# Performance work log

Hardware: AMD Instinct MI355X
Metric: run time of the kernel (lower is better)

## Reference

```python
import jax, jax.numpy as jnp
from jax import lax
import numpy as np

K = 8          # local window radius -> (2K+1)^2 = 289 offsets
TOPK = 256     # topk channels kept for fg/bg correlation
EPS = 1e-5     # torch InstanceNorm2d default eps


def _conv3(x, w, b):
    # 3x3 conv, stride 1, pad 1, NCHW/OIHW
    y = lax.conv_general_dilated(x, w, (1, 1), ((1, 1), (1, 1)),
                                 dimension_numbers=('NCHW', 'OIHW', 'NCHW'))
    return y + b[None, :, None, None]


def _inorm(x):
    # InstanceNorm2d(affine=False): per (b,c) normalization over HxW, biased var
    m = jnp.mean(x, axis=(2, 3), keepdims=True)
    v = jnp.mean((x - m) ** 2, axis=(2, 3), keepdims=True)
    return (x - m) * lax.rsqrt(v + EPS)


def _aic(x, w1, b1, w2, b2):
    # AIC(in, hidden): conv3x3(in->hidden)+IN+ReLU -> conv3x3(hidden->in)+IN+ReLU
    h = jax.nn.relu(_inorm(_conv3(x, w1, b1)))
    return jax.nn.relu(_inorm(_conv3(h, w2, b2)))


def _amaxpool(x, H, W):
    # adaptive_max_pool2d with exact integer factor (384/48 = 8)
    kh, kw = x.shape[2] // H, x.shape[3] // W
    return lax.reduce_window(x, -jnp.inf, lax.max, (1, 1, kh, kw), (1, 1, kh, kw), 'VALID')


def _topk_c(x, k=TOPK):
    # topk over channel axis, values sorted descending (matches torch.topk)
    v, _ = lax.top_k(jnp.transpose(x, (0, 2, 3, 1)), k)  # [B,H,W,k]
    return jnp.transpose(v, (0, 3, 1, 2))                 # [B,k,H,W]


def _resize_ac(x, H, W):
    # bilinear interpolate, align_corners=True
    B, C, h, w = x.shape
    def grid(n_out, n_in):
        if n_out == 1:
            return jnp.zeros((1,), jnp.float32)
        return jnp.arange(n_out, dtype=jnp.float32) * ((n_in - 1) / (n_out - 1))
    ys, xs = grid(H, h), grid(W, w)
    y0 = jnp.clip(jnp.floor(ys).astype(jnp.int32), 0, h - 1)
    y1 = jnp.minimum(y0 + 1, h - 1)
    x0 = jnp.clip(jnp.floor(xs).astype(jnp.int32), 0, w - 1)
    x1 = jnp.minimum(x0 + 1, w - 1)
    wy = (ys - y0.astype(jnp.float32))[None, None, :, None]
    wx = (xs - x0.astype(jnp.float32))[None, None, None, :]
    rows = x[:, :, y0, :] * (1.0 - wy) + x[:, :, y1, :] * wy  # [B,C,H,w]
    return rows[:, :, :, x0] * (1.0 - wx) + rows[:, :, :, x1] * wx


def _forward(p3, p2, p1, kg1, klp, key_mask, pre_mask,
             conv_top_w, conv_top_b,
             aic_top_w1, aic_top_b1, aic_top_w2, aic_top_b2,
             r1a_w1, r1a_b1, r1a_w2, r1a_b2,
             r1b_w1, r1b_b1, r1b_w2, r1b_b2,
             r2a_w1, r2a_b1, r2a_w2, r2a_b2,
             r2b_w1, r2b_b1, r2b_w2, r2b_b2,
             dec_conv1_w, dec_conv1_b, pred_w, pred_b):
    B, _, H, W = kg1.shape  # kg1: [B, H*W, H, W]
    # --- Global, mode=2: fg/bg topk over the global correlation volume ---
    gm = _amaxpool(key_mask, H, W).reshape(B, H * W, 1, 1)
    gf = _topk_c(kg1 * gm)
    gb = _topk_c(kg1 * (1.0 - gm))
    # --- Local, mode=2: unfold mask into 17x17 windows, fg/bg topk ---
    lm = _amaxpool(pre_mask, H, W)                       # [B,1,H,W]
    lmp = jnp.pad(lm, ((0, 0), (0, 0), (K, K), (K, K)))  # zero pad (FF.pad default)
    patches = lax.conv_general_dilated_patches(
        lmp, (2 * K + 1, 2 * K + 1), (1, 1), 'VALID',
        dimension_numbers=('NCHW', 'OIHW', 'NCHW'))      # [B,289,H,W], ch = dy*17+dx
    lf = _topk_c(klp * patches)
    lb = _topk_c(klp * (1.0 - patches))
    # --- fuse at p3 resolution ---
    pm = _amaxpool(pre_mask, H, W)
    x = jnp.concatenate([p3, gf, gb, lf, lb, pm], axis=1)  # [B, 256*5+1, H, W]
    x = _conv3(x, conv_top_w, conv_top_b)                  # 1281 -> 256
    x = _aic(x, aic_top_w1, aic_top_b1, aic_top_w2, aic_top_b2)
    # --- Decoder: Refine(256,64) -> conv 256->64 -> Refine(64,64) -> pred ---
    y = _resize_ac(x, p2.shape[2], p2.shape[3])
    y = _aic(y, r1a_w1, r1a_b1, r1a_w2, r1a_b2)
    y = y + p2
    y = _aic(y, r1b_w1, r1b_b1, r1b_w2, r1b_b2)
    y = _conv3(y, dec_conv1_w, dec_conv1_b)
    z = _resize_ac(y, p1.shape[2], p1.shape[3])
    z = _aic(z, r2a_w1, r2a_b1, r2a_w2, r2a_b2)
    z = z + p1
    z = _aic(z, r2b_w1, r2b_b1, r2b_w2, r2b_b2)
    return jax.nn.sigmoid(_conv3(z, pred_w, pred_b))       # [B,1,192,192]


def setup_inputs() -> dict:
    key = jax.random.key(0)
    ks = jax.random.split(key, 40)
    B, H, W = 2, 48, 48
    inp = {}
    inp['p3'] = jax.random.normal(ks[0], (B, 256, H, W), jnp.float32)
    inp['p2'] = jax.random.normal(ks[1], (B, 256, 2 * H, 2 * W), jnp.float32)
    inp['p1'] = jax.random.normal(ks[2], (B, 64, 4 * H, 4 * W), jnp.float32)
    inp['kg1'] = jax.random.normal(ks[3], (B, H * W, H, W), jnp.float32)
    inp['klp'] = jax.random.normal(ks[4], (B, (2 * K + 1) ** 2, H, W), jnp.float32)
    inp['key_mask'] = jax.random.uniform(ks[5], (B, 1, 8 * H, 8 * W), dtype=jnp.float32)
    inp['pre_mask'] = jax.random.uniform(ks[6], (B, 1, 8 * H, 8 * W), dtype=jnp.float32)
    i = [7]
    def p(shape, s=0.05):
        w = jax.random.normal(ks[i[0]], shape, jnp.float32) * s
        i[0] += 1
        return w
    inp['conv_top_w'] = p((256, 256 * 5 + 1, 3, 3))
    inp['conv_top_b'] = jnp.zeros((256,), jnp.float32)
    for nm, (ci, ch) in [('aic_top', (256, 64)), ('r1a', (256, 64)), ('r1b', (256, 64)),
                         ('r2a', (64, 64)), ('r2b', (64, 64))]:
        inp[nm + '_w1'] = p((ch, ci, 3, 3)); inp[nm + '_b1'] = jnp.zeros((ch,), jnp.float32)
        inp[nm + '_w2'] = p((ci, ch, 3, 3)); inp[nm + '_b2'] = jnp.zeros((ci,), jnp.float32)
    inp['dec_conv1_w'] = p((64, 256, 3, 3)); inp['dec_conv1_b'] = jnp.zeros((64,), jnp.float32)
    inp['pred_w'] = p((1, 64, 3, 3)); inp['pred_b'] = jnp.zeros((1,), jnp.float32)
    return inp


def reference(p3, p2, p1, kg1, klp, key_mask, pre_mask,
              conv_top_w, conv_top_b,
              aic_top_w1, aic_top_b1, aic_top_w2, aic_top_b2,
              r1a_w1, r1a_b1, r1a_w2, r1a_b2,
              r1b_w1, r1b_b1, r1b_w2, r1b_b2,
              r2a_w1, r2a_b1, r2a_w2, r2a_b2,
              r2b_w1, r2b_b1, r2b_w2, r2b_b2,
              dec_conv1_w, dec_conv1_b, pred_w, pred_b):
    return _forward(p3, p2, p1, kg1, klp, key_mask, pre_mask,
                    conv_top_w, conv_top_b,
                    aic_top_w1, aic_top_b1, aic_top_w2, aic_top_b2,
                    r1a_w1, r1a_b1, r1a_w2, r1a_b2,
                    r1b_w1, r1b_b1, r1b_w2, r1b_b2,
                    r2a_w1, r2a_b1, r2a_w2, r2a_b2,
                    r2b_w1, r2b_b1, r2b_w2, r2b_b2,
                    dec_conv1_w, dec_conv1_b, pred_w, pred_b)
```

## Files before the change

### kernel.cpp

```cpp
#include <hip/hip_runtime.h>
#include <math.h>

#define TPB 256

typedef _Float16 h8 __attribute__((ext_vector_type(8)));
typedef float f4 __attribute__((ext_vector_type(4)));
typedef unsigned short ushort_t;

__device__ __forceinline__ unsigned short f2bf(float x) {
  unsigned int u = __float_as_uint(x);
  unsigned int r = (u + 0x7fffu + ((u >> 16) & 1u)) >> 16;
  return (unsigned short)r;
}
__device__ __forceinline__ float bf2f(unsigned short h) {
  return __uint_as_float(((unsigned int)h) << 16);
}
__device__ __forceinline__ ushort_t f2h(float x) {
  _Float16 h = (_Float16)x;
  return *(ushort_t*)&h;
}
__device__ __forceinline__ float h2f(ushort_t u) {
  _Float16 h = *(_Float16*)&u;
  return (float)h;
}
__device__ __forceinline__ unsigned key16_of(float x) {
  unsigned h = (unsigned)f2h(x);
  return h ^ ((h >> 15) ? 0xFFFFu : 0x8000u);
}
__device__ __forceinline__ ushort_t un_key16(unsigned k) {
  return (ushort_t)(k ^ ((k & 0x8000u) ? 0x8000u : 0xFFFFu));
}

__global__ __launch_bounds__(TPB) void pool8_kernel(const float* __restrict__ in,
                                                    float* __restrict__ out, int total) {
  int idx = blockIdx.x * TPB + threadIdx.x;
  if (idx >= total) return;
  int b = idx / 2304, yx = idx - b * 2304;
  int y = yx / 48, x = yx - y * 48;
  const float* p = in + ((size_t)b * 384 + (size_t)y * 8) * 384 + (size_t)x * 8;
  float m = -INFINITY;
#pragma unroll
  for (int i = 0; i < 8; ++i)
#pragma unroll
    for (int j = 0; j < 8; ++j) m = fmaxf(m, p[(size_t)i * 384 + j]);
  out[idx] = m;
}

__global__ __launch_bounds__(TPB) void tposef_kernel(const float* __restrict__ src,
                                                     float* __restrict__ dst, int C, int HW,
                                                     int DS) {
  __shared__ float tile[64][65];
  int px0 = blockIdx.x * 64;
  int c0 = blockIdx.y * 64;
  int b = blockIdx.z;
  int tid = threadIdx.x;
#pragma unroll
  for (int i = 0; i < 16; ++i) {
    int c = (tid >> 6) + i * 4, p = tid & 63;
    tile[c][p] = src[((size_t)b * C + c0 + c) * HW + px0 + p];
  }
  __syncthreads();
#pragma unroll
  for (int i = 0; i < 16; ++i) {
    int c = tid & 63, p = (tid >> 6) + i * 4;
    dst[((size_t)b * HW + px0 + p) * DS + c0 + c] = tile[c][p];
  }
}

__global__ __launch_bounds__(TPB) void tposeg_kernel(const float* __restrict__ src,
                                                     float* __restrict__ dst, int C, int HW,
                                                     int DS) {
  __shared__ float tile[64][65];
  int px0 = blockIdx.x * 64;
  int c0 = blockIdx.y * 64;
  int b = blockIdx.z;
  int tid = threadIdx.x;
#pragma unroll
  for (int i = 0; i < 16; ++i) {
    int c = (tid >> 6) + i * 4, p = tid & 63;
    float v = 0.f;
    if (c0 + c < C) v = src[((size_t)b * C + c0 + c) * HW + px0 + p];
    tile[c][p] = v;
  }
  __syncthreads();
#pragma unroll
  for (int i = 0; i < 16; ++i) {
    int c = tid & 63, p = (tid >> 6) + i * 4;
    if (c0 + c < C)
      dst[((size_t)b * HW + px0 + p) * DS + c0 + c] = tile[c][p];
  }
}

__global__ __launch_bounds__(TPB) void tposeh_kernel(const float* __restrict__ src,
                                                     ushort_t* __restrict__ dst, int C, int HW,
                                                     int DS) {
  __shared__ float tile[64][65];
  int px0 = blockIdx.x * 64;
  int c0 = blockIdx.y * 64;
  int b = blockIdx.z;
  int tid = threadIdx.x;
#pragma unroll
  for (int i = 0; i < 16; ++i) {
    int c = (tid >> 6) + i * 4, p = tid & 63;
    tile[c][p] = src[((size_t)b * C + c0 + c) * HW + px0 + p];
  }
  __syncthreads();
#pragma unroll
  for (int i = 0; i < 16; ++i) {
    int c = tid & 63, p = (tid >> 6) + i * 4;
    dst[((size_t)b * HW + px0 + p) * DS + c0 + c] = f2h(tile[c][p]);
  }
}

__global__ __launch_bounds__(TPB) void topk_global_kernel(const float* __restrict__ kgT,
                                                          const float* __restrict__ gm,
                                                          ushort_t* __restrict__ xcat) {
  __shared__ unsigned hist[4][256];
  __shared__ ushort_t sout[256];
  __shared__ unsigned selT[1], selA[1];
  __shared__ unsigned cntG[1], cntE[1];
  const int tid = threadIdx.x;
  const int lane = tid & 63, wid = tid >> 6;
  const int fb = blockIdx.x;
  int bid = blockIdx.y;
  int b = bid / 2304, yx = bid - b * 2304;
  const float* kp = kgT + ((size_t)b * 2304 + yx) * 2304;
  const float* gp = gm + (size_t)b * 2304;
  unsigned kk9[9];
#pragma unroll
  for (int j = 0; j < 9; ++j) {
    int i = tid + 256 * j;
    float v = kp[i];
    float g = gp[i];
    kk9[j] = key16_of(v * (fb ? (1.0f - g) : g));
  }
#pragma unroll
  for (int w = 0; w < 4; ++w) hist[w][tid] = 0;
  __syncthreads();
#pragma unroll
  for (int j = 0; j < 9; ++j) atomicAdd(&hist[wid][kk9[j] >> 8], 1u);
  __syncthreads();
  if (wid == 0) {
    unsigned h0 = hist[0][4 * lane] + hist[1][4 * lane] + hist[2][4 * lane] +
                  hist[3][4 * lane];
    unsigned h1 = hist[0][4 * lane + 1] + hist[1][4 * lane + 1] + hist[2][4 * lane + 1] +
                  hist[3][4 * lane + 1];
    unsigned h2 = hist[0][4 * lane + 2] + hist[1][4 * lane + 2] + hist[2][4 * lane + 2] +
                  hist[3][4 * lane + 2];
    unsigned h3 = hist[0][4 * lane + 3] + hist[1][4 * lane + 3] + hist[2][4 * lane + 3] +
                  hist[3][4 * lane + 3];
    unsigned x = h0 + h1 + h2 + h3;
#pragma unroll
    for (int d = 1; d < 64; d <<= 1) {
      unsigned y = __shfl_down(x, d, 64);
      if (lane + d < 64) x += y;
    }
    unsigned long long m = __ballot(x >= 256u);
    int tl = 63 - __clzll(m);
    if (lane == tl) {
      unsigned s1 = x - h0, s2 = s1 - h1, s3 = s2 - h2, s4 = s3 - h3;
      int jj;
      unsigned A;
      if (s3 >= 256u) { jj = 3; A = s4; }
      else if (s2 >= 256u) { jj = 2; A = s3; }
      else if (s1 >= 256u) { jj = 1; A = s2; }
      else { jj = 0; A = s1; }
      selT[0] = 4 * tl + jj;
      selA[0] = A;
    }
  }
  __syncthreads();
  const unsigned T0 = selT[0], gt0 = selA[0];
  const unsigned K1 = 256u - gt0;
  hist[0][tid] = 0;
  __syncthreads();
#pragma unroll
  for (int j = 0; j < 9; ++j)
    if ((kk9[j] >> 8) == T0) atomicAdd(&hist[0][kk9[j] & 0xFFu], 1u);
  __syncthreads();
  if (wid == 0) {
    unsigned h0 = hist[0][4 * lane], h1 = hist[0][4 * lane + 1];
    unsigned h2 = hist[0][4 * lane + 2], h3 = hist[0][4 * lane + 3];
    unsigned x = h0 + h1 + h2 + h3;
#pragma unroll
    for (int d = 1; d < 64; d <<= 1) {
      unsigned y = __shfl_down(x, d, 64);
      if (lane + d < 64) x += y;
    }
    unsigned long long m = __ballot(x >= K1);
    int tl = 63 - __clzll(m);
    if (lane == tl) {
      unsigned s1 = x - h0, s2 = s1 - h1, s3 = s2 - h2, s4 = s3 - h3;
      int jj;
      unsigned A;
      if (s3 >= K1) { jj = 3; A = s4; }
      else if (s2 >= K1) { jj = 2; A = s3; }
      else if (s1 >= K1) { jj = 1; A = s2; }
      else { jj = 0; A = s1; }
      selT[0] = 4 * tl + jj;
      selA[0] = A;
    }
  }
  __syncthreads();
  const unsigned tK = (T0 << 8) | selT[0];
  const unsigned nGT = gt0 + selA[0], need = 256u - nGT;
  if (tid == 0) { cntG[0] = 0; cntE[0] = 0; }
  __syncthreads();
#pragma unroll
  for (int j = 0; j < 9; ++j) {
    unsigned k = kk9[j];
    if (k > tK) sout[atomicAdd(&cntG[0], 1u)] = (ushort_t)k;
    else if (k == tK) {
      unsigned e = atomicAdd(&cntE[0], 1u);
      if (e < need) sout[nGT + e] = (ushort_t)tK;
    }
  }
  __syncthreads();
  if (wid == 0) {
    for (int kk = 2; kk <= 256; kk <<= 1) {
      for (int j = kk >> 1; j > 0; j >>= 1) {
#pragma unroll
        for (int r = 0; r < 2; ++r) {
          int p = lane + r * 64;
          int t = (p & (j - 1)) | ((p & ~(j - 1)) << 1);
          int ixj = t | j;
          bool up = ((t & kk) == 0);
          ushort_t a = sout[t], c = sout[ixj];
          if (up ? (a > c) : (a < c)) { sout[t] = c; sout[ixj] = a; }
        }
        __builtin_amdgcn_wave_barrier();
      }
    }
  }
  __syncthreads();
  size_t base = ((size_t)(b * 2304 + yx)) * 1312 + (fb ? 512 : 256);
  xcat[base + tid] = un_key16((unsigned)sout[255 - tid]);
}

__global__ __launch_bounds__(TPB) void topk_local_kernel(const float* __restrict__ klpT,
                                                         const float* __restrict__ lm,
                                                         ushort_t* __restrict__ xcat) {
  const int lane = threadIdx.x & 63;
  const int wid = threadIdx.x >> 6;
  const int pix = blockIdx.x * 2 + (wid >> 1);
  const int fb = wid & 1;
  const int b = pix / 2304;
  const int yx = pix - b * 2304;
  const int y = yx / 48, x = yx - y * 48;
  const float* kp = klpT + (size_t)pix * 320;
  float v8[8];
#pragma unroll
  for (int r = 0; r < 8; ++r) {
    int i = r * 64 + lane;
    float vv = -INFINITY;
    if (i < 289) {
      int dy = i / 17, dx = i - dy * 17;
      int sy = y + dy - 8, sx = x + dx - 8;
      float pv = 0.f;
      if (sy >= 0 && sy < 48 && sx >= 0 && sx < 48) pv = lm[(size_t)b * 2304 + sy * 48 + sx];
      float v = kp[i];
      vv = v * (fb ? (1.0f - pv) : pv);
    }
    v8[r] = vv;
  }
  for (int k = 2; k <= 512; k <<= 1) {
    for (int j = k >> 1; j > 0; j >>= 1) {
      if (j >= 64) {
        const int jr = j >> 6;
#pragma unroll
        for (int r = 0; r < 8; ++r) {
          if ((r & jr) == 0) {
            const int rp = r | jr;
            bool up = (((unsigned)(r * 64) & (unsigned)k) == 0);
            float a = v8[r], c = v8[rp];
            if (up) {
              v8[r] = fminf(a, c); v8[rp] = fmaxf(a, c);
            } else {
              v8[r] = fmaxf(a, c); v8[rp] = fminf(a, c);
            }
          }
        }
      } else {
        bool lower = ((lane & j) == 0);
#pragma unroll
        for (int r = 0; r < 8; ++r) {
          float p = __shfl_xor(v8[r], j, 64);
          bool up = (((unsigned)(r * 64 + lane) & (unsigned)k) == 0);
          bool takeMin = (lower == up);
          v8[r] = takeMin ? fminf(v8[r], p) : fmaxf(v8[r], p);
        }
      }
    }
  }
  size_t base = (size_t)pix * 1312 + (fb ? 1024 : 768);
#pragma unroll
  for (int r = 4; r < 8; ++r) {
    int t = 511 - (r * 64 + lane);
    xcat[base + t] = f2h(v8[r]);
  }
}

__global__ __launch_bounds__(TPB) void pm_pad_kernel(const float* __restrict__ lm,
                                                     ushort_t* __restrict__ xcat) {
  int idx = blockIdx.x * TPB + threadIdx.x;
  if (idx >= 2 * 2304 * 32) return;
  int ch = idx & 31;
  int r = idx >> 5;
  xcat[(size_t)r * 1312 + 1280 + ch] = (ch == 0) ? f2h(lm[r]) : (ushort_t)0;
}

struct WallDesc {
  const float* src[13];
  int CinW[13], CIP[13], CoutPad[13], CoutReal[13];
  unsigned start[14];
  int n;
};
__global__ __launch_bounds__(TPB) void wconv_all_kernel(WallDesc D, ushort_t* __restrict__ whi,
                                                        int total) {
  int i = blockIdx.x * TPB + threadIdx.x;
  if (i >= total) return;
  int k = 0;
  while (k + 1 < D.n && (unsigned)i >= D.start[k + 1]) ++k;
  int j = i - D.start[k];
  int e = j & 7;
  int t = j >> 3;
  int l16 = t & 15; t >>= 4;
  int h4 = t & 3; t >>= 2;
  int NCOG = D.CoutPad[k] >> 4;
  int cog = t % NCOG; t /= NCOG;
  int kykx = t % 9;
  int chunk = t / 9;
  int co = cog * 16 + l16;
  int ci = chunk * 32 + h4 * 8 + e;
  float v = 0.f;
  if (ci < D.CinW[k] && co < D.CoutReal[k])
    v = D.src[k][((size_t)co * D.CinW[k] + ci) * 9 + kykx];
  whi[i] = f2h(v);
}

template <int NORM>
__device__ __forceinline__ uint4 norm8(uint4 v, const float* __restrict__ nmean,
                                       const float* __restrict__ ninv,
                                       const void* __restrict__ nres, size_t mb,
                                       size_t pxoff) {
  float f[8];
  f[0] = h2f((ushort_t)(v.x & 0xffff)); f[1] = h2f((ushort_t)(v.x >> 16));
  f[2] = h2f((ushort_t)(v.y & 0xffff)); f[3] = h2f((ushort_t)(v.y >> 16));
  f[4] = h2f((ushort_t)(v.z & 0xffff)); f[5] = h2f((ushort_t)(v.z >> 16));
  f[6] = h2f((ushort_t)(v.w & 0xffff)); f[7] = h2f((ushort_t)(v.w >> 16));
  float4 m0 = *(const float4*)(nmean + mb);
  float4 m1 = *(const float4*)(nmean + mb + 4);
  float4 i0 = *(const float4*)(ninv + mb);
  float4 i1 = *(const float4*)(ninv + mb + 4);
  float o[8];
  o[0] = fmaxf((f[0] - m0.x) * i0.x, 0.f);
  o[1] = fmaxf((f[1] - m0.y) * i0.y, 0.f);
  o[2] = fmaxf((f[2] - m0.z) * i0.z, 0.f);
  o[3] = fmaxf((f[3] - m0.w) * i0.w, 0.f);
  o[4] = fmaxf((f[4] - m1.x) * i1.x, 0.f);
  o[5] = fmaxf((f[5] - m1.y) * i1.y, 0.f);
  o[6] = fmaxf((f[6] - m1.z) * i1.z, 0.f);
  o[7] = fmaxf((f[7] - m1.w) * i1.w, 0.f);
  if (NORM == 2) {
    uint4 rv = *(const uint4*)((const ushort_t*)nres + pxoff);
    o[0] += h2f((ushort_t)(rv.x & 0xffff)); o[1] += h2f((ushort_t)(rv.x >> 16));
    o[2] += h2f((ushort_t)(rv.y & 0xffff)); o[3] += h2f((ushort_t)(rv.y >> 16));
    o[4] += h2f((ushort_t)(rv.z & 0xffff)); o[5] += h2f((ushort_t)(rv.z >> 16));
    o[6] += h2f((ushort_t)(rv.w & 0xffff)); o[7] += h2f((ushort_t)(rv.w >> 16));
  } else if (NORM == 3) {
    const float* rp = (const float*)nres + pxoff;
    float4 r0 = *(const float4*)rp;
    float4 r1 = *(const float4*)(rp + 4);
    o[0] += r0.x; o[1] += r0.y; o[2] += r0.z; o[3] += r0.w;
    o[4] += r1.x; o[5] += r1.y; o[6] += r1.z; o[7] += r1.w;
  }
  uint4 out;
  out.x = (unsigned)f2h(o[0]) | ((unsigned)f2h(o[1]) << 16);
  out.y = (unsigned)f2h(o[2]) | ((unsigned)f2h(o[3]) << 16);
  out.z = (unsigned)f2h(o[4]) | ((unsigned)f2h(o[5]) << 16);
  out.w = (unsigned)f2h(o[6]) | ((unsigned)f2h(o[7]) << 16);
  return out;
}

template <int MFR, int ACT, int STAT, int GEOM, int NORM>
__global__ __launch_bounds__(TPB) void conv_mfma_kernel(
    const ushort_t* __restrict__ in, const ushort_t* __restrict__ whi,
    const float* __restrict__ bias,
    ushort_t* __restrict__ outh, float* __restrict__ outf, ushort_t* __restrict__ partial,
    float* __restrict__ stat, int ntiles,
    const float* __restrict__ nmean, const float* __restrict__ ninv,
    const void* __restrict__ nres,
    int hin, int win, float rs,
    int CIP, int Cout, int H, int W, int S, int ci_per_s) {
  const int NPIX = (GEOM == 1) ? 100 : 180;
  const int PITCH = 10;
  __shared__ uint4 sB[(GEOM == 1) ? 800 : 1440];
  const int MB = (GEOM == 1) ? 64 : MFR * 32;
  const int tid = threadIdx.x;
  const int lane = tid & 63;
  const int lo16 = lane & 15, hi4 = lane >> 4;
  const int wid = tid >> 6;
  const int wco = (GEOM == 1) ? wid : (wid & 1);
  const int wpx = (GEOM == 1) ? 0 : (wid >> 1);
  const int tilesX = W >> 3;
  const int tx0 = (blockIdx.x % tilesX) << 3;
  const int ty0 = (blockIdx.x / tilesX) << ((GEOM == 1) ? 3 : 4);
  const int s = blockIdx.y % S;
  const int co0 = (blockIdx.y / S) * MB;
  const int b = blockIdx.z;
  const int NCOG = Cout >> 4;
  const size_t HW = (size_t)H * W;
  const ushort_t* inb = in + (size_t)b * HW * CIP;
  const ushort_t* srcb = in + (size_t)b * hin * win * CIP;
  int ci_begin = s * ci_per_s;
  int ci_end = ci_begin + ci_per_s;
  if (ci_end > CIP) ci_end = CIP;
  f4 acc[MFR][4];
#pragma unroll
  for (int m = 0; m < MFR; ++m)
#pragma unroll
    for (int n = 0; n < 4; ++n) acc[m][n] = (f4){0.f, 0.f, 0.f, 0.f};

  for (int ci0 = ci_begin; ci0 < ci_end; ci0 += 64) {
    const bool has2 = (ci0 + 32 < ci_end);
    __syncthreads();
#pragma unroll
    for (int it = 0; it < 6; ++it) {
      int u = it * TPB + tid;
      if (u < NPIX * 8) {
        int q4 = u / NPIX;
        int pix = u - q4 * NPIX;
        int prow = pix / PITCH, pcol = pix - prow * PITCH;
        int gy = ty0 - 1 + prow, gx = tx0 - 1 + pcol;
        int ci = ci0 + q4 * 8;
        bool inbp = (ci < CIP && gy >= 0 && gy < H && gx >= 0 && gx < W);
        uint4 v = {0u, 0u, 0u, 0u};
        if (inbp) {
          if (NORM <= 3) {
            v = *(const uint4*)(inb + ((size_t)gy * W + gx) * CIP + ci);
            if (NORM != 0) {
              size_t mb = (size_t)b * CIP + ci;
              size_t pxoff = ((size_t)b * HW + (size_t)gy * W + gx) * CIP + ci;
              v = norm8<NORM>(v, nmean, ninv, nres, mb, pxoff);
            }
          } else {
            float ys = gy * rs, xs = gx * rs;
            int y0 = (int)floorf(ys);
            if (y0 > hin - 1) y0 = hin - 1;
            int x0 = (int)floorf(xs);
            if (x0 > win - 1) x0 = win - 1;
            int y1 = y0 + 1 < hin ? y0 + 1 : hin - 1;
            int x1 = x0 + 1 < win ? x0 + 1 : win - 1;
            float wy = ys - (float)y0, wx = xs - (float)x0;
            uint4 s00 = *(const uint4*)(srcb + ((size_t)y0 * win + x0) * CIP + ci);
            uint4 s01 = *(const uint4*)(srcb + ((size_t)y0 * win + x1) * CIP + ci);
            uint4 s10 = *(const uint4*)(srcb + ((size_t)y1 * win + x0) * CIP + ci);
            uint4 s11 = *(const uint4*)(srcb + ((size_t)y1 * win + x1) * CIP + ci);
            float w00 = (1.f - wy) * (1.f - wx), w01 = (1.f - wy) * wx;
            float w10 = wy * (1.f - wx), w11 = wy * wx;
            union U8 { uint4 q; ushort_t sv[8]; };
            U8 u00, u01, u10, u11, uo;
            u00.q = s00; u01.q = s01; u10.q = s10; u11.q = s11;
#pragma unroll
            for (int k8 = 0; k8 < 8; ++k8) {
              float val = h2f(u00.sv[k8]) * w00 + h2f(u01.sv[k8]) * w01 +
                          h2f(u10.sv[k8]) * w10 + h2f(u11.sv[k8]) * w11;
              uo.sv[k8] = f2h(val);
            }
            v = uo.q;
          }
        }
        sB[q4 * NPIX + pix] = v;
      }
    }
    __syncthreads();
#pragma unroll
    for (int h = 0; h < 2; ++h) {
      if (h == 1 && !has2) continue;
      const int chunkIdx = (ci0 >> 5) + h;
#pragma unroll
      for (int ky = 0; ky < 3; ++ky) {
#pragma unroll
        for (int kx = 0; kx < 3; ++kx) {
          const int kykx = ky * 3 + kx;
          h8 ah[MFR];
#pragma unroll
          for (int m = 0; m < MFR; ++m) {
            int cog = (co0 + wco * (GEOM == 1 ? 16 : (MB / 2)) + m * 16) >> 4;
            size_t woff = (((size_t)chunkIdx * 9 + kykx) * NCOG + cog) * 512 + (size_t)lane * 8;
            ah[m] = *(const h8*)(whi + woff);
          }
          h8 bf[4];
#pragma unroll
          for (int n = 0; n < 4; ++n) {
            int pix = (wpx * 8 + n * 2 + (lo16 >> 3) + ky) * PITCH + (lo16 & 7) + kx;
            union { uint4 q; h8 v; } ub;
            ub.q = sB[(h * 4 + hi4) * NPIX + pix];
            bf[n] = ub.v;
          }
#pragma unroll
          for (int m = 0; m < MFR; ++m)
#pragma unroll
            for (int n = 0; n < 4; ++n)
              acc[m][n] = __builtin_amdgcn_mfma_f32_16x16x32_f16(ah[m], bf[n], acc[m][n], 0, 0, 0);
        }
      }
    }
  }

#pragma unroll
  for (int m = 0; m < MFR; ++m) {
#pragma unroll
    for (int n = 0; n < 4; ++n) {
      int py = ty0 + wpx * 8 + n * 2 + (lo16 >> 3);
      int pxx = tx0 + (lo16 & 7);
      int co_r0 = co0 + wco * (GEOM == 1 ? 16 : (MB / 2)) + m * 16 + hi4 * 4;
      if (ACT == 1) {
        if (wco == 0 && m == 0 && hi4 == 0) {
          float v = acc[0][n][0] + bias[0];
          outf[(size_t)b * HW + (size_t)py * W + pxx] = 1.0f / (1.0f + expf(-v));
        }
      } else if (S == 1) {
        float4 bv = *(const float4*)(bias + co_r0);
        unsigned w0 = (unsigned)f2h(acc[m][n][0] + bv.x) |
                      ((unsigned)f2h(acc[m][n][1] + bv.y) << 16);
        unsigned w1 = (unsigned)f2h(acc[m][n][2] + bv.z) |
                      ((unsigned)f2h(acc[m][n][3] + bv.w) << 16);
        uint2 o = {w0, w1};
        *(uint2*)(outh + (((size_t)b * HW + (size_t)py * W + pxx) * Cout + co_r0)) = o;
        if (STAT) {
          acc[m][n][0] = h2f((ushort_t)(w0 & 0xffff));
          acc[m][n][1] = h2f((ushort_t)(w0 >> 16));
          acc[m][n][2] = h2f((ushort_t)(w1 & 0xffff));
          acc[m][n][3] = h2f((ushort_t)(w1 >> 16));
        }
      } else {
        uint2 o;
        o.x = (unsigned)f2h(acc[m][n][0]) | ((unsigned)f2h(acc[m][n][1]) << 16);
        o.y = (unsigned)f2h(acc[m][n][2]) | ((unsigned)f2h(acc[m][n][3]) << 16);
        *(uint2*)(partial + (((size_t)(s * 2 + b) * HW + (size_t)py * W + pxx) * Cout + co_r0)) = o;
      }
    }
  }

  if (STAT) {
    __syncthreads();
    f4* lredS = (f4*)sB;
    f4* lredQ = lredS + 32;
    if (GEOM == 1) {
      f4 sv = acc[0][0] + acc[0][1] + acc[0][2] + acc[0][3];
      f4 qv = acc[0][0] * acc[0][0] + acc[0][1] * acc[0][1] + acc[0][2] * acc[0][2] +
              acc[0][3] * acc[0][3];
#pragma unroll
      for (int off = 1; off < 16; off <<= 1) {
#pragma unroll
        for (int kq = 0; kq < 4; ++kq) {
          sv[kq] += __shfl_xor(sv[kq], off, 64);
          qv[kq] += __shfl_xor(qv[kq], off, 64);
        }
      }
      if (lo16 == 0) {
        lredS[wid * 4 + hi4] = sv;
        lredQ[wid * 4 + hi4] = qv;
      }
      __syncthreads();
      if (tid < 16) {
        int widT = tid >> 2, h4T = tid & 3;
        int c = co0 + widT * 16 + h4T * 4;
        size_t sbase = ((size_t)b * ntiles + blockIdx.x) * (size_t)(Cout * 2);
        *(f4*)(stat + sbase + c) = lredS[tid];
        *(f4*)(stat + sbase + Cout + c) = lredQ[tid];
      }
    } else {
#pragma unroll
      for (int m = 0; m < MFR; ++m) {
        f4 sv = acc[m][0] + acc[m][1] + acc[m][2] + acc[m][3];
        f4 qv = acc[m][0] * acc[m][0] + acc[m][1] * acc[m][1] + acc[m][2] * acc[m][2] +
                acc[m][3] * acc[m][3];
#pragma unroll
        for (int off = 1; off < 16; off <<= 1) {
#pragma unroll
          for (int kq = 0; kq < 4; ++kq) {
            sv[kq] += __shfl_xor(sv[kq], off, 64);
            qv[kq] += __shfl_xor(qv[kq], off, 64);
          }
        }
        if (lo16 == 0) {
          lredS[(wid * MFR + m) * 4 + hi4] = sv;
          lredQ[(wid * MFR + m) * 4 + hi4] = qv;
        }
      }
      __syncthreads();
      if (tid < 2 * MFR * 4) {
        int wcoT = tid / (MFR * 4);
        int r = tid % (MFR * 4);
        int mT = r / 4;
        int h4T = r % 4;
        f4 sv = lredS[((wcoT)*MFR + mT) * 4 + h4T] + lredS[((wcoT + 2) * MFR + mT) * 4 + h4T];
        f4 qv = lredQ[((wcoT)*MFR + mT) * 4 + h4T] + lredQ[((wcoT + 2) * MFR + mT) * 4 + h4T];
        int c = co0 + wcoT * (MB / 2) + mT * 16 + h4T * 4;
        size_t sbase = ((size_t)b * ntiles + blockIdx.x) * (size_t)(Cout * 2);
        *(f4*)(stat + sbase + c) = sv;
        *(f4*)(stat + sbase + Cout + c) = qv;
      }
    }
  }
}

__global__ __launch_bounds__(TPB) void pred_kernel(const ushort_t* __restrict__ in,
                                                   const float* __restrict__ w,
                                                   const float* __restrict__ bias,
                                                   const float* __restrict__ nmean,
                                                   const float* __restrict__ ninv,
                                                   float* __restrict__ outp) {
  __shared__ uint4 hal[324 * 9];
  __shared__ float wl[576];
  const int tid = threadIdx.x;
  const int tx0 = (blockIdx.x % 12) * 16;
  const int ty0 = (blockIdx.x / 12) * 16;
  const int b = blockIdx.y;
  const ushort_t* inb = in + (size_t)b * 36864 * 64;
  for (int u = tid; u < 576; u += TPB) {
    int ci = u & 63, kk = u >> 6;
    wl[u] = w[(size_t)ci * 9 + kk];
  }
  for (int u = tid; u < 2592; u += TPB) {
    int px = u >> 3, q4 = u & 7;
    int r = px / 18, c = px - r * 18;
    int gy = ty0 - 1 + r, gx = tx0 - 1 + c;
    uint4 v = {0u, 0u, 0u, 0u};
    if (gy >= 0 && gy < 192 && gx >= 0 && gx < 192) {
      v = *(const uint4*)(inb + ((size_t)gy * 192 + gx) * 64 + q4 * 8);
      v = norm8<1>(v, nmean, ninv, nullptr, (size_t)b * 64 + q4 * 8, 0);
    }
    hal[px * 9 + q4] = v;
  }
  __syncthreads();
  const int ty = tid >> 4, tx = tid & 15;
  float acc = bias[0];
#pragma unroll
  for (int ky = 0; ky < 3; ++ky) {
#pragma unroll
    for (int kx = 0; kx < 3; ++kx) {
      int base = ((ty + ky) * 18 + tx + kx) * 9;
      const float* wp = &wl[(ky * 3 + kx) * 64];
#pragma unroll
      for (int q = 0; q < 8; ++q) {
        uint4 v = hal[base + q];
        const float* w8 = wp + q * 8;
        acc = fmaf(h2f((ushort_t)(v.x & 0xffff)), w8[0], acc);
        acc = fmaf(h2f((ushort_t)(v.x >> 16)), w8[1], acc);
        acc = fmaf(h2f((ushort_t)(v.y & 0xffff)), w8[2], acc);
        acc = fmaf(h2f((ushort_t)(v.y >> 16)), w8[3], acc);
        acc = fmaf(h2f((ushort_t)(v.z & 0xffff)), w8[4], acc);
        acc = fmaf(h2f((ushort_t)(v.z >> 16)), w8[5], acc);
        acc = fmaf(h2f((ushort_t)(v.w & 0xffff)), w8[6], acc);
        acc = fmaf(h2f((ushort_t)(v.w >> 16)), w8[7], acc);
      }
    }
  }
  outp[(size_t)b * 36864 + (size_t)(ty0 + ty) * 192 + (tx0 + tx)] =
      1.0f / (1.0f + expf(-acc));
}

template <int STAT>
__global__ __launch_bounds__(TPB) void reduce_nhwc_kernel(const ushort_t* __restrict__ partial,
                                                          const float* __restrict__ bias,
                                                          ushort_t* __restrict__ outh,
                                                          float* __restrict__ stat, int bpb,
                                                          int S, int Cout, int HW, int total4) {
  int i = blockIdx.x * TPB + threadIdx.x;
  float4 accv = {0.f, 0.f, 0.f, 0.f};
  unsigned w0 = 0, w1 = 0;
  int e = i * 4;
  int CHW = Cout * HW;
  if (i < total4) {
    int b = e / CHW;
    int rem = e - b * CHW;
    int co = e % Cout;
    for (int ss = 0; ss < S; ++ss) {
      const uint2 t2 = *(const uint2*)(partial + (size_t)(ss * 2 + b) * CHW + rem);
      accv.x += h2f((ushort_t)(t2.x & 0xffff));
      accv.y += h2f((ushort_t)(t2.x >> 16));
      accv.z += h2f((ushort_t)(t2.y & 0xffff));
      accv.w += h2f((ushort_t)(t2.y >> 16));
    }
    float4 bv = *(const float4*)(bias + co);
    w0 = (unsigned)f2h(accv.x + bv.x) | ((unsigned)f2h(accv.y + bv.y) << 16);
    w1 = (unsigned)f2h(accv.z + bv.z) | ((unsigned)f2h(accv.w + bv.w) << 16);
    uint2 o = {w0, w1};
    *(uint2*)(outh + (size_t)b * CHW + rem) = o;
  }
  if (STAT) {
    __shared__ f4 ls[4][16], lq[4][16];
    const int tid = threadIdx.x;
    const int lane = tid & 63, wv = tid >> 6;
    f4 r;
    r[0] = h2f((ushort_t)(w0 & 0xffff));
    r[1] = h2f((ushort_t)(w0 >> 16));
    r[2] = h2f((ushort_t)(w1 & 0xffff));
    r[3] = h2f((ushort_t)(w1 >> 16));
    f4 sv = r;
    f4 qv = r * r;
#pragma unroll
    for (int kq = 0; kq < 4; ++kq) {
      sv[kq] += __shfl_down(sv[kq], 16, 64);
      qv[kq] += __shfl_down(qv[kq], 16, 64);
      sv[kq] += __shfl_down(sv[kq], 32, 64);
      qv[kq] += __shfl_down(qv[kq], 32, 64);
    }
    if (lane < 16) {
      ls[wv][lane] = sv;
      lq[wv][lane] = qv;
    }
    __syncthreads();
    if (tid < 16) {
      f4 S4 = ls[0][tid] + ls[1][tid] + ls[2][tid] + ls[3][tid];
      f4 Q4 = lq[0][tid] + lq[1][tid] + lq[2][tid] + lq[3][tid];
      int b = (blockIdx.x * (TPB * 4)) / CHW;
      int tblk = blockIdx.x - b * bpb;
      int c = tid * 4;
      size_t sbase = ((size_t)b * bpb + tblk) * (size_t)(Cout * 2);
      *(f4*)(stat + sbase + c) = S4;
      *(f4*)(stat + sbase + Cout + c) = Q4;
    }
  }
}

__global__ __launch_bounds__(TPB) void in_stats_kernel(const ushort_t* __restrict__ x,
                                                       float* __restrict__ stat, int N, int C) {
  __shared__ float ls[4][64], lq[4][64];
  int CG = C >> 6;
  int b = blockIdx.x / CG, cg = blockIdx.x % CG;
  int slice = blockIdx.y;
  int c = threadIdx.x & 63, p = threadIdx.x >> 6;
  int cnt = N >> 6;
  int base = slice * cnt;
  float s = 0.f, q = 0.f;
  const ushort_t* xp = x + ((size_t)b * N) * C + cg * 64 + c;
  for (int px = base + p; px < base + cnt; px += 4) {
    float v = h2f(xp[(size_t)px * C]);
    s += v;
    q = fmaf(v, v, q);
  }
  ls[p][c] = s;
  lq[p][c] = q;
  __syncthreads();
  if (threadIdx.x < 64) {
    float S = ls[0][threadIdx.x] + ls[1][threadIdx.x] + ls[2][threadIdx.x] + ls[3][threadIdx.x];
    float Q = lq[0][threadIdx.x] + lq[1][threadIdx.x] + lq[2][threadIdx.x] + lq[3][threadIdx.x];
    int Ctot = 2 * C;
    int idx = b * C + cg * 64 + threadIdx.x;
    stat[(size_t)(slice * Ctot + idx) * 2] = S;
    stat[(size_t)(slice * Ctot + idx) * 2 + 1] = Q;
  }
}

__global__ __launch_bounds__(TPB) void in_final_kernel(const float* __restrict__ stat,
                                                       float* __restrict__ mean,
                                                       float* __restrict__ inv, int N, int Ctot) {
  int idx = blockIdx.x * TPB + threadIdx.x;
  if (idx >= Ctot) return;
  float S = 0.f, Q = 0.f;
  for (int sl = 0; sl < 64; ++sl) {
    S += stat[(size_t)(sl * Ctot + idx) * 2];
    Q += stat[(size_t)(sl * Ctot + idx) * 2 + 1];
  }
  float m = S / (float)N;
  float var = Q / (float)N - m * m;
  if (var < 0.f) var = 0.f;
  mean[idx] = m;
  inv[idx] = 1.0f / sqrtf(var + 1e-5f);
}

__global__ __launch_bounds__(TPB) void in_final_tiles_kernel(const float* __restrict__ stat,
                                                             float* __restrict__ mean,
                                                             float* __restrict__ inv, int N,
                                                             int C, int ntiles) {
  __shared__ float rs_[TPB], rq_[TPB];
  int idx = blockIdx.x;
  int b = idx / C, c = idx % C;
  float S = 0.f, Q = 0.f;
  for (int t = threadIdx.x; t < ntiles; t += TPB) {
    size_t base = ((size_t)b * ntiles + t) * (size_t)(C * 2);
    S += stat[base + c];
    Q += stat[base + C + c];
  }
  rs_[threadIdx.x] = S;
  rq_[threadIdx.x] = Q;
  __syncthreads();
  for (int off = TPB / 2; off > 0; off >>= 1) {
    if (threadIdx.x < off) {
      rs_[threadIdx.x] += rs_[threadIdx.x + off];
      rq_[threadIdx.x] += rq_[threadIdx.x + off];
    }
    __syncthreads();
  }
  if (threadIdx.x == 0) {
    float ma = rs_[0] / (float)N;
    float var = rq_[0] / (float)N - ma * ma;
    if (var < 0.f) var = 0.f;
    mean[idx] = ma;
    inv[idx] = 1.0f / sqrtf(var + 1e-5f);
  }
}

template <int NORM>
__global__ __launch_bounds__(TPB) void resize4_kernel(const ushort_t* __restrict__ in,
                                                      ushort_t* __restrict__ out,
                                                      const float* __restrict__ nmean,
                                                      const float* __restrict__ ninv, int C,
                                                      int hin, int win, int Hout, int Wout,
                                                      float r, int total4) {
  for (int i = blockIdx.x * TPB + threadIdx.x; i < total4; i += gridDim.x * TPB) {
    int e = i * 4;
    int c = e % C;
    int t = e / C;
    int X = t % Wout;
    int t2 = t / Wout;
    int Y = t2 % Hout;
    int b = t2 / Hout;
    float ys = Y * r, xs = X * r;
    int y0 = (int)floorf(ys);
    if (y0 > hin - 1) y0 = hin - 1;
    int x0 = (int)floorf(xs);
    if (x0 > win - 1) x0 = win - 1;
    int y1 = y0 + 1 < hin ? y0 + 1 : hin - 1;
    int x1 = x0 + 1 < win ? x0 + 1 : win - 1;
    float wy = ys - (float)y0, wx = xs - (float)x0;
    const ushort_t* ip = in + ((size_t)b * hin * win) * C + c;
    uint2 a2 = *(const uint2*)(ip + ((size_t)y0 * win + x0) * C);
    uint2 b2 = *(const uint2*)(ip + ((size_t)y0 * win + x1) * C);
    uint2 c2 = *(const uint2*)(ip + ((size_t)y1 * win + x0) * C);
    uint2 d2 = *(const uint2*)(ip + ((size_t)y1 * win + x1) * C);
    float av[4], bv[4], cv[4], dv[4];
    av[0] = h2f((ushort_t)(a2.x & 0xffff)); av[1] = h2f((ushort_t)(a2.x >> 16));
    av[2] = h2f((ushort_t)(a2.y & 0xffff)); av[3] = h2f((ushort_t)(a2.y >> 16));
    bv[0] = h2f((ushort_t)(b2.x & 0xffff)); bv[1] = h2f((ushort_t)(b2.x >> 16));
    bv[2] = h2f((ushort_t)(b2.y & 0xffff)); bv[3] = h2f((ushort_t)(b2.y >> 16));
    cv[0] = h2f((ushort_t)(c2.x & 0xffff)); cv[1] = h2f((ushort_t)(c2.x >> 16));
    cv[2] = h2f((ushort_t)(c2.y & 0xffff)); cv[3] = h2f((ushort_t)(c2.y >> 16));
    dv[0] = h2f((ushort_t)(d2.x & 0xffff)); dv[1] = h2f((ushort_t)(d2.x >> 16));
    dv[2] = h2f((ushort_t)(d2.y & 0xffff)); dv[3] = h2f((ushort_t)(d2.y >> 16));
    if (NORM) {
      float4 m4 = *(const float4*)(nmean + (size_t)b * C + c);
      float4 i4 = *(const float4*)(ninv + (size_t)b * C + c);
      float mm[4] = {m4.x, m4.y, m4.z, m4.w};
      float ii[4] = {i4.x, i4.y, i4.z, i4.w};
#pragma unroll
      for (int k = 0; k < 4; ++k) {
        av[k] = fmaxf((av[k] - mm[k]) * ii[k], 0.f);
        bv[k] = fmaxf((bv[k] - mm[k]) * ii[k], 0.f);
        cv[k] = fmaxf((cv[k] - mm[k]) * ii[k], 0.f);
        dv[k] = fmaxf((dv[k] - mm[k]) * ii[k], 0.f);
      }
    }
    float w00 = (1.f - wy) * (1.f - wx), w01 = (1.f - wy) * wx;
    float w10 = wy * (1.f - wx), w11 = wy * wx;
    float o[4];
#pragma unroll
    for (int k = 0; k < 4; ++k)
      o[k] = av[k] * w00 + bv[k] * w01 + cv[k] * w10 + dv[k] * w11;
    uint2 ov;
    ov.x = (unsigned)f2h(o[0]) | ((unsigned)f2h(o[1]) << 16);
    ov.y = (unsigned)f2h(o[2]) | ((unsigned)f2h(o[3]) << 16);
    *(uint2*)(out + e) = ov;
  }
}

extern "C" void kernel_launch(void* const* d_in, const int* in_sizes, int n_in,
                              void* d_out, int out_size, void* d_ws, size_t ws_size,
                              hipStream_t stream) {
  (void)in_sizes; (void)n_in; (void)out_size;
  const float* p3 = (const float*)d_in[0];
  const float* p2 = (const float*)d_in[1];
  const float* p1 = (const float*)d_in[2];
  const float* kg1 = (const float*)d_in[3];
  const float* klp = (const float*)d_in[4];
  const float* key_mask = (const float*)d_in[5];
  const float* pre_mask = (const float*)d_in[6];
  const float* conv_top_w = (const float*)d_in[7];
  const float* conv_top_b = (const float*)d_in[8];
  const float* aic_top_w1 = (const float*)d_in[9];
  const float* aic_top_b1 = (const float*)d_in[10];
  const float* aic_top_w2 = (const float*)d_in[11];
  const float* aic_top_b2 = (const float*)d_in[12];
  const float* r1a_w1 = (const float*)d_in[13];
  const float* r1a_b1 = (const float*)d_in[14];
  const float* r1a_w2 = (const float*)d_in[15];
  const float* r1a_b2 = (const float*)d_in[16];
  const float* r1b_w1 = (const float*)d_in[17];
  const float* r1b_b1 = (const float*)d_in[18];
  const float* r1b_w2 = (const float*)d_in[19];
  const float* r1b_b2 = (const float*)d_in[20];
  const float* r2a_w1 = (const float*)d_in[21];
  const float* r2a_b1 = (const float*)d_in[22];
  const float* r2a_w2 = (const float*)d_in[23];
  const float* r2a_b2 = (const float*)d_in[24];
  const float* r2b_w1 = (const float*)d_in[25];
  const float* r2b_b1 = (const float*)d_in[26];
  const float* r2b_w2 = (const float*)d_in[27];
  const float* r2b_b2 = (const float*)d_in[28];
  const float* dec_w = (const float*)d_in[29];
  const float* dec_b = (const float*)d_in[30];
  const float* pred_w = (const float*)d_in[31];
  const float* pred_b = (const float*)d_in[32];
  float* outp = (float*)d_out;

  const size_t OFF_GM = 0;
  const size_t OFF_LM = 4608;
  const size_t OFF_STAT = 9216;
  const size_t OFF_MEAN = 304128;
  const size_t OFF_INV = 304640;
  const size_t OFF_WB = 305152;
  const size_t OFF_AH0 = 4544512;
  const size_t OFF_AH1 = 7567360;
  const size_t OFF_AH2 = 8157184;
  const size_t OFF_AH3 = 8304640;
  const size_t OFF_AH4 = 8894464;
  const size_t OFF_AH5 = 11253760;
  const size_t OFF_P1T = 13613056;
  const size_t OFF_P2T = 18331648;
  const size_t TOTAL_F = 19511296;
  if (ws_size < TOTAL_F * sizeof(float)) return;

  float* ws = (float*)d_ws;
  float* gm = ws + OFF_GM;
  float* lm = ws + OFF_LM;
  float* statb = ws + OFF_STAT;
  float* meanb = ws + OFF_MEAN;
  float* invb = ws + OFF_INV;
  ushort_t* wbh = (ushort_t*)(ws + OFF_WB);
  ushort_t* xcat_h = (ushort_t*)(ws + OFF_AH0);
  ushort_t* y96_h = (ushort_t*)(ws + OFF_AH0);
  ushort_t* a0_h = (ushort_t*)(ws + OFF_AH1);
  ushort_t* h96_h = (ushort_t*)(ws + OFF_AH1);
  ushort_t* d96_h = (ushort_t*)(ws + OFF_AH1);
  ushort_t* h48_h = (ushort_t*)(ws + OFF_AH2);
  ushort_t* a1_h = (ushort_t*)(ws + OFF_AH3);
  ushort_t* R1_h = (ushort_t*)(ws + OFF_AH4);
  ushort_t* zA_h = (ushort_t*)(ws + OFF_AH4);
  ushort_t* R0_h = (ushort_t*)(ws + OFF_AH5);
  ushort_t* zB_h = (ushort_t*)(ws + OFF_AH5);
  ushort_t* Pbuf16 = (ushort_t*)(ws + OFF_P1T);
  ushort_t* PbufTop16 = (ushort_t*)(ws + OFF_AH4);
  float* p1t = ws + OFF_P1T;
  ushort_t* p2t = (ushort_t*)(ws + OFF_P2T);
  float* kgT = ws + OFF_AH4;
  float* klpT = ws + OFF_P1T;

  WallDesc D;
  const float* wsrc[13] = {conv_top_w, aic_top_w1, aic_top_w2, r1a_w1, r1a_w2, r1b_w1,
                           r1b_w2, dec_w, r2a_w1, r2a_w2, r2b_w1, r2b_w2, pred_w};
  const int wcin[13] = {1281, 256, 64, 256, 64, 256, 64, 256, 64, 64, 64, 64, 64};
  const int wcip[13] = {1312, 256, 64, 256, 64, 256, 64, 256, 64, 64, 64, 64, 64};
  const int wcop[13] = {256, 64, 256, 64, 256, 64, 256, 64, 64, 64, 64, 64, 64};
  const int wcor[13] = {256, 64, 256, 64, 256, 64, 256, 64, 64, 64, 64, 64, 1};
  unsigned cum = 0;
  unsigned woff[13];
  for (int k = 0; k < 13; ++k) {
    D.src[k] = wsrc[k];
    D.CinW[k] = wcin[k];
    D.CIP[k] = wcip[k];
    D.CoutPad[k] = wcop[k];
    D.CoutReal[k] = wcor[k];
    D.start[k] = cum;
    woff[k] = cum;
    cum += (unsigned)(wcop[k] * 9 * wcip[k]);
  }
  D.start[13] = cum;
  D.n = 13;
  wconv_all_kernel<<<(cum + TPB - 1) / TPB, TPB, 0, stream>>>(D, wbh, (int)cum);

  pool8_kernel<<<(2 * 2304 + TPB - 1) / TPB, TPB, 0, stream>>>(key_mask, gm, 2 * 2304);
  pool8_kernel<<<(2 * 2304 + TPB - 1) / TPB, TPB, 0, stream>>>(pre_mask, lm, 2 * 2304);
  tposeg_kernel<<<dim3(36, 5, 2), TPB, 0, stream>>>(klp, klpT, 289, 2304, 320);
  topk_local_kernel<<<2304, TPB, 0, stream>>>(klpT, lm, xcat_h);
  tposef_kernel<<<dim3(36, 36, 2), TPB, 0, stream>>>(kg1, kgT, 2304, 2304, 2304);
  topk_global_kernel<<<dim3(2, 2 * 2304), TPB, 0, stream>>>(kgT, gm, xcat_h);
  tposeh_kernel<<<dim3(36, 4, 2), TPB, 0, stream>>>(p3, xcat_h, 256, 2304, 1312);
  pm_pad_kernel<<<(2 * 2304 * 32 + TPB - 1) / TPB, TPB, 0, stream>>>(lm, xcat_h);

  auto conv = [&](const ushort_t* src, int wk, const float* bb, ushort_t* dsth,
                  ushort_t* part, int CIP, int CoutPad, int H, int W, int S, int MB,
                  int geom, int redStat, int normMode, const void* res, int hin, int win,
                  float rsc) {
    const ushort_t* whiK = wbh + woff[wk];
    int chunks = CIP / 32;
    int cps = ((chunks + S - 1) / S) * 32;
    if (geom == 1) {
      int ntiles = (W / 8) * (H / 8);
      dim3 grid(ntiles, CoutPad / 64, 2);
      if (normMode == 1)
        conv_mfma_kernel<1, 0, 1, 1, 1><<<grid, TPB, 0, stream>>>(
            src, whiK, bb, dsth, nullptr, nullptr, statb, ntiles, meanb, invb, res,
            hin, win, rsc, CIP, CoutPad, H, W, 1, cps);
      else if (normMode == 3)
        conv_mfma_kernel<1, 0, 1, 1, 3><<<grid, TPB, 0, stream>>>(
            src, whiK, bb, dsth, nullptr, nullptr, statb, ntiles, meanb, invb, res,
            hin, win, rsc, CIP, CoutPad, H, W, 1, cps);
      else if (normMode == 5)
        conv_mfma_kernel<1, 0, 1, 1, 5><<<grid, TPB, 0, stream>>>(
            src, whiK, bb, dsth, nullptr, nullptr, statb, ntiles, meanb, invb, res,
            hin, win, rsc, CIP, CoutPad, H, W, 1, cps);
      else
        conv_mfma_kernel<1, 0, 1, 1, 0><<<grid, TPB, 0, stream>>>(
            src, whiK, bb, dsth, nullptr, nullptr, statb, ntiles, meanb, invb, res,
            hin, win, rsc, CIP, CoutPad, H, W, 1, cps);
      return;
    }
    int ntiles = (W / 8) * (H / 16);
    dim3 grid(ntiles, (CoutPad / MB) * S, 2);
    if (MB == 128)
      conv_mfma_kernel<4, 0, 0, 0, 0><<<grid, TPB, 0, stream>>>(
          src, whiK, bb, dsth, nullptr, part, nullptr, 0, meanb, invb, res, hin, win,
          rsc, CIP, CoutPad, H, W, S, cps);
    else if (normMode == 1)
      conv_mfma_kernel<2, 0, 0, 0, 1><<<grid, TPB, 0, stream>>>(
          src, whiK, bb, dsth, nullptr, part, nullptr, 0, meanb, invb, res, hin, win,
          rsc, CIP, CoutPad, H, W, S, cps);
    else if (normMode == 2)
      conv_mfma_kernel<2, 0, 0, 0, 2><<<grid, TPB, 0, stream>>>(
          src, whiK, bb, dsth, nullptr, part, nullptr, 0, meanb, invb, res, hin, win,
          rsc, CIP, CoutPad, H, W, S, cps);
    else
      conv_mfma_kernel<2, 0, 0, 0, 0><<<grid, TPB, 0, stream>>>(
          src, whiK, bb, dsth, nullptr, part, nullptr, 0, meanb, invb, res, hin, win,
          rsc, CIP, CoutPad, H, W, S, cps);
    if (S > 1) {
      int HW = H * W;
      int total4 = 2 * CoutPad * HW / 4;
      int nblk = (total4 + TPB - 1) / TPB;
      int bpb = (CoutPad * HW) / (TPB * 4);
      if (redStat)
        reduce_nhwc_kernel<1><<<nblk, TPB, 0, stream>>>(part, bb, dsth, statb, bpb, S,
                                                        CoutPad, HW, total4);
      else
        reduce_nhwc_kernel<0><<<nblk, TPB, 0, stream>>>(part, bb, dsth, nullptr, 0, S,
                                                        CoutPad, HW, total4);
    }
  };
  auto stats_plain = [&](ushort_t* x, int C, int N) {
    dim3 g1(2 * (C / 64), 64);
    in_stats_kernel<<<g1, TPB, 0, stream>>>(x, statb, N, C);
    int Ctot = 2 * C;
    in_final_kernel<<<(Ctot + TPB - 1) / TPB, TPB, 0, stream>>>(statb, meanb, invb, N, Ctot);
  };
  auto stats_tiles = [&](int C, int N, int ntiles) {
    in_final_tiles_kernel<<<2 * C, TPB, 0, stream>>>(statb, meanb, invb, N, C, ntiles);
  };

  conv(xcat_h, 0, conv_top_b, a0_h, PbufTop16, 1312, 256, 48, 48, 7, 128, 0, 0, 0, nullptr,
       48, 48, 1.f);
  conv(a0_h, 1, aic_top_b1, h48_h, Pbuf16, 256, 64, 48, 48, 8, 64, 0, 1, 0, nullptr, 48, 48,
       1.f);
  stats_tiles(64, 2304, 144);
  conv(h48_h, 2, aic_top_b2, a1_h, Pbuf16, 64, 256, 48, 48, 2, 64, 0, 0, 1, nullptr, 48, 48,
       1.f);
  stats_plain(a1_h, 256, 2304);

  {
    int total4 = 2 * 96 * 96 * 256 / 4;
    int g = (total4 + TPB - 1) / TPB; if (g > 4096) g = 4096;
    resize4_kernel<1><<<g, TPB, 0, stream>>>(a1_h, y96_h, meanb, invb, 256, 48, 48, 96, 96,
                                             47.f / 95.f, total4);
  }
  conv(y96_h, 3, r1a_b1, h96_h, Pbuf16, 256, 64, 96, 96, 4, 64, 0, 1, 0, nullptr, 96, 96,
       1.f);
  tposeh_kernel<<<dim3(144, 4, 2), TPB, 0, stream>>>(p2, p2t, 256, 9216, 256);
  stats_tiles(64, 9216, 576);
  conv(h96_h, 4, r1a_b2, R1_h, nullptr, 64, 256, 96, 96, 1, 64, 1, 0, 1, nullptr, 96, 96,
       1.f);
  stats_tiles(256, 9216, 144);
  conv(R1_h, 5, r1b_b1, h96_h, Pbuf16, 256, 64, 96, 96, 4, 64, 0, 1, 2, p2t, 96, 96, 1.f);
  stats_tiles(64, 9216, 576);
  conv(h96_h, 6, r1b_b2, R0_h, nullptr, 64, 256, 96, 96, 1, 64, 1, 0, 1, nullptr, 96, 96,
       1.f);
  stats_tiles(256, 9216, 144);
  conv(R0_h, 7, dec_b, d96_h, Pbuf16, 256, 64, 96, 96, 4, 64, 0, 0, 1, nullptr, 96, 96,
       1.f);
  tposef_kernel<<<dim3(576, 1, 2), TPB, 0, stream>>>(p1, p1t, 64, 36864, 64);

  conv(d96_h, 8, r2a_b1, zA_h, nullptr, 64, 64, 192, 192, 1, 64, 1, 0, 5, nullptr, 96, 96,
       95.f / 191.f);
  stats_tiles(64, 36864, 576);
  conv(zA_h, 9, r2a_b2, zB_h, nullptr, 64, 64, 192, 192, 1, 64, 1, 0, 1, nullptr, 192, 192,
       1.f);
  stats_tiles(64, 36864, 576);
  conv(zB_h, 10, r2b_b1, zA_h, nullptr, 64, 64, 192, 192, 1, 64, 1, 0, 3, p1t, 192, 192,
       1.f);
  stats_tiles(64, 36864, 576);
  conv(zA_h, 11, r2b_b2, zB_h, nullptr, 64, 64, 192, 192, 1, 64, 1, 0, 1, nullptr, 192, 192,
       1.f);
  stats_tiles(64, 36864, 576);

  pred_kernel<<<dim3(144, 2), TPB, 0, stream>>>(zB_h, pred_w, pred_b, meanb, invb, outp);
}
```

Measured before the change: 531.9 us.

## Run global top-k selection per wavefront instead of per block

The global top-k kernel now gives each 64-lane wavefront its own (pixel, fg/bg) task, with a private histogram, selection state and sort buffer. This replaces block-wide __syncthreads with wave barriers and removes the phases where three waves sat idle during scans and the bitonic sort. The grid shrinks from 9216 blocks to 2304 blocks of four tasks each. In exchange each lane holds 36 keys in registers instead of 9, which may raise register pressure, and the shared-memory atomics within a wave may contend more.

```diff
diff --git a/kernel.cpp b/kernel.cpp
--- a/kernel.cpp
+++ b/kernel.cpp
@@ -116,39 +116,35 @@
                                                           const float* __restrict__ gm,
                                                           ushort_t* __restrict__ xcat) {
   __shared__ unsigned hist[4][256];
-  __shared__ ushort_t sout[256];
-  __shared__ unsigned selT[1], selA[1];
-  __shared__ unsigned cntG[1], cntE[1];
-  const int tid = threadIdx.x;
-  const int lane = tid & 63, wid = tid >> 6;
-  const int fb = blockIdx.x;
-  int bid = blockIdx.y;
-  int b = bid / 2304, yx = bid - b * 2304;
+  __shared__ ushort_t sout[4][256];
+  __shared__ unsigned selT[4], selA[4];
+  __shared__ unsigned cntG[4], cntE[4];
+  const int lane = threadIdx.x & 63;
+  const int wid = threadIdx.x >> 6;
+  const int task = blockIdx.x * 4 + wid;
+  const int pix = task >> 1;
+  const int fb = task & 1;
+  const int b = pix / 2304, yx = pix - b * 2304;
   const float* kp = kgT + ((size_t)b * 2304 + yx) * 2304;
   const float* gp = gm + (size_t)b * 2304;
-  unsigned kk9[9];
-#pragma unroll
-  for (int j = 0; j < 9; ++j) {
-    int i = tid + 256 * j;
+  unsigned kk[36];
+#pragma unroll
+  for (int e = 0; e < 36; ++e) {
+    int i = e * 64 + lane;
     float v = kp[i];
     float g = gp[i];
-    kk9[j] = key16_of(v * (fb ? (1.0f - g) : g));
-  }
-#pragma unroll
-  for (int w = 0; w < 4; ++w) hist[w][tid] = 0;
-  __syncthreads();
-#pragma unroll
-  for (int j = 0; j < 9; ++j) atomicAdd(&hist[wid][kk9[j] >> 8], 1u);
-  __syncthreads();
-  if (wid == 0) {
-    unsigned h0 = hist[0][4 * lane] + hist[1][4 * lane] + hist[2][4 * lane] +
-                  hist[3][4 * lane];
-    unsigned h1 = hist[0][4 * lane + 1] + hist[1][4 * lane + 1] + hist[2][4 * lane + 1] +
-                  hist[3][4 * lane + 1];
-    unsigned h2 = hist[0][4 * lane + 2] + hist[1][4 * lane + 2] + hist[2][4 * lane + 2] +
-                  hist[3][4 * lane + 2];
-    unsigned h3 = hist[0][4 * lane + 3] + hist[1][4 * lane + 3] + hist[2][4 * lane + 3] +
-                  hist[3][4 * lane + 3];
+    kk[e] = key16_of(v * (fb ? (1.0f - g) : g));
+  }
+  unsigned* h = hist[wid];
+#pragma unroll
+  for (int q = 0; q < 4; ++q) h[lane * 4 + q] = 0;
+  __builtin_amdgcn_wave_barrier();
+#pragma unroll
+  for (int e = 0; e < 36; ++e) atomicAdd(&h[kk[e] >> 8], 1u);
+  __builtin_amdgcn_wave_barrier();
+  {
+    unsigned h0 = h[4 * lane], h1 = h[4 * lane + 1];
+    unsigned h2 = h[4 * lane + 2], h3 = h[4 * lane + 3];
     unsigned x = h0 + h1 + h2 + h3;
 #pragma unroll
     for (int d = 1; d < 64; d <<= 1) {
@@ -165,22 +161,23 @@
       else if (s2 >= 256u) { jj = 2; A = s3; }
       else if (s1 >= 256u) { jj = 1; A = s2; }
       else { jj = 0; A = s1; }
-      selT[0] = 4 * tl + jj;
-      selA[0] = A;
-    }
-  }
-  __syncthreads();
-  const unsigned T0 = selT[0], gt0 = selA[0];
+      selT[wid] = 4 * tl + jj;
+      selA[wid] = A;
+    }
+  }
+  __builtin_amdgcn_wave_barrier();
+  const unsigned T0 = selT[wid], gt0 = selA[wid];
   const unsigned K1 = 256u - gt0;
-  hist[0][tid] = 0;
-  __syncthreads();
-#pragma unroll
-  for (int j = 0; j < 9; ++j)
-    if ((kk9[j] >> 8) == T0) atomicAdd(&hist[0][kk9[j] & 0xFFu], 1u);
-  __syncthreads();
-  if (wid == 0) {
-    unsigned h0 = hist[0][4 * lane], h1 = hist[0][4 * lane + 1];
-    unsigned h2 = hist[0][4 * lane + 2], h3 = hist[0][4 * lane + 3];
+#pragma unroll
+  for (int q = 0; q < 4; ++q) h[lane * 4 + q] = 0;
+  __builtin_amdgcn_wave_barrier();
+#pragma unroll
+  for (int e = 0; e < 36; ++e)
+    if ((kk[e] >> 8) == T0) atomicAdd(&h[kk[e] & 0xFFu], 1u);
+  __builtin_amdgcn_wave_barrier();
+  {
+    unsigned h0 = h[4 * lane], h1 = h[4 * lane + 1];
+    unsigned h2 = h[4 * lane + 2], h3 = h[4 * lane + 3];
     unsigned x = h0 + h1 + h2 + h3;
 #pragma unroll
     for (int d = 1; d < 64; d <<= 1) {
@@ -197,44 +194,46 @@
       else if (s2 >= K1) { jj = 2; A = s3; }
       else if (s1 >= K1) { jj = 1; A = s2; }
       else { jj = 0; A = s1; }
-      selT[0] = 4 * tl + jj;
-      selA[0] = A;
-    }
-  }
-  __syncthreads();
-  const unsigned tK = (T0 << 8) | selT[0];
-  const unsigned nGT = gt0 + selA[0], need = 256u - nGT;
-  if (tid == 0) { cntG[0] = 0; cntE[0] = 0; }
-  __syncthreads();
-#pragma unroll
-  for (int j = 0; j < 9; ++j) {
-    unsigned k = kk9[j];
-    if (k > tK) sout[atomicAdd(&cntG[0], 1u)] = (ushort_t)k;
+      selT[wid] = 4 * tl + jj;
+      selA[wid] = A;
+    }
+  }
+  __builtin_amdgcn_wave_barrier();
+  const unsigned tK = (T0 << 8) | selT[wid];
+  const unsigned nGT = gt0 + selA[wid], need = 256u - nGT;
+  if (lane == 0) { cntG[wid] = 0; cntE[wid] = 0; }
+  __builtin_amdgcn_wave_barrier();
+  ushort_t* sarr = sout[wid];
+#pragma unroll
+  for (int e = 0; e < 36; ++e) {
+    unsigned k = kk[e];
+    if (k > tK) sarr[atomicAdd(&cntG[wid], 1u)] = (ushort_t)k;
     else if (k == tK) {
-      unsigned e = atomicAdd(&cntE[0], 1u);
-      if (e < need) sout[nGT + e] = (ushort_t)tK;
-    }
-  }
-  __syncthreads();
-  if (wid == 0) {
-    for (int kk = 2; kk <= 256; kk <<= 1) {
-      for (int j = kk >> 1; j > 0; j >>= 1) {
-#pragma unroll
-        for (int r = 0; r < 2; ++r) {
-          int p = lane + r * 64;
-          int t = (p & (j - 1)) | ((p & ~(j - 1)) << 1);
-          int ixj = t | j;
-          bool up = ((t & kk) == 0);
-          ushort_t a = sout[t], c = sout[ixj];
-          if (up ? (a > c) : (a < c)) { sout[t] = c; sout[ixj] = a; }
-        }
-        __builtin_amdgcn_wave_barrier();
-      }
-    }
-  }
-  __syncthreads();
-  size_t base = ((size_t)(b * 2304 + yx)) * 1312 + (fb ? 512 : 256);
-  xcat[base + tid] = un_key16((unsigned)sout[255 - tid]);
+      unsigned ee = atomicAdd(&cntE[wid], 1u);
+      if (ee < need) sarr[nGT + ee] = (ushort_t)tK;
+    }
+  }
+  __builtin_amdgcn_wave_barrier();
+  for (int kkk = 2; kkk <= 256; kkk <<= 1) {
+    for (int j = kkk >> 1; j > 0; j >>= 1) {
+#pragma unroll
+      for (int r = 0; r < 2; ++r) {
+        int p = lane + r * 64;
+        int t = (p & (j - 1)) | ((p & ~(j - 1)) << 1);
+        int ixj = t | j;
+        bool up = ((t & kkk) == 0);
+        ushort_t a = sarr[t], c = sarr[ixj];
+        if (up ? (a > c) : (a < c)) { sarr[t] = c; sarr[ixj] = a; }
+      }
+      __builtin_amdgcn_wave_barrier();
+    }
+  }
+  size_t base = ((size_t)pix) * 1312 + (fb ? 512 : 256);
+#pragma unroll
+  for (int r = 0; r < 4; ++r) {
+    int t = lane + r * 64;
+    xcat[base + t] = un_key16((unsigned)sarr[255 - t]);
+  }
 }
 
 __global__ __launch_bounds__(TPB) void topk_local_kernel(const float* __restrict__ klpT,
@@ -977,7 +976,7 @@
   tposeg_kernel<<<dim3(36, 5, 2), TPB, 0, stream>>>(klp, klpT, 289, 2304, 320);
   topk_local_kernel<<<2304, TPB, 0, stream>>>(klpT, lm, xcat_h);
   tposef_kernel<<<dim3(36, 36, 2), TPB, 0, stream>>>(kg1, kgT, 2304, 2304, 2304);
-  topk_global_kernel<<<dim3(2, 2 * 2304), TPB, 0, stream>>>(kgT, gm, xcat_h);
+  topk_global_kernel<<<2304, TPB, 0, stream>>>(kgT, gm, xcat_h);
   tposeh_kernel<<<dim3(36, 4, 2), TPB, 0, stream>>>(p3, xcat_h, 256, 2304, 1312);
   pm_pad_kernel<<<(2 * 2304 * 32 + TPB - 1) / TPB, TPB, 0, stream>>>(lm, xcat_h);
 
```

Result: faster. 513.9 us (-3.4%).
